# Kernel optimization log

Measured on AMD Instinct MI355X. Metric: run time of the kernel, lower is better.

Reference implementation:

```python
import jax, jax.numpy as jnp
import numpy as np

N = 100000   # nodes
E = 1600000  # edges (before self-loops)
F = 128      # in_dim
C = 32       # hidden_dim
H1 = 2       # heads of gat1
G = 64       # graphs in batch
NEG = 0.2    # leaky_relu slope (PyG default)


def segment_softmax(s, idx, num):
    # softmax of s grouped by idx (PyG `softmax`), s: [E, ...], idx: [E]
    m = jax.ops.segment_max(s, idx, num_segments=num)
    m = jnp.where(jnp.isfinite(m), m, 0.0)  # empty segments -> 0 baseline
    e = jnp.exp(s - m[idx])
    d = jax.ops.segment_sum(e, idx, num_segments=num)
    return e / (d[idx] + 1e-16)


def gatv2_layer(x, src, dst, Wl, bl, Wr, br, att, bias, heads, ch):
    # Faithful PyG GATv2Conv (share_weights=False, concat=True)
    n = x.shape[0]
    xl = (x @ Wl + bl).reshape(n, heads, ch)  # source transform
    xr = (x @ Wr + br).reshape(n, heads, ch)  # target transform
    e = jax.nn.leaky_relu(xl[src] + xr[dst], NEG)       # [E, H, C]
    alpha = jnp.sum(e * att, axis=-1)                    # [E, H]
    alpha = segment_softmax(alpha, dst, n)               # softmax over incoming edges
    out = jax.ops.segment_sum(alpha[..., None] * xl[src], dst, num_segments=n)
    return out.reshape(n, heads * ch) + bias


def setup_inputs() -> dict:
    key = jax.random.key(0)
    ks = jax.random.split(key, 24)
    s = 0.1
    inp = {
        "x": jax.random.normal(ks[0], (N, F), jnp.float32),
        "edge_index": jax.random.randint(ks[1], (2, E), 0, N),
        "batch": jnp.sort(jax.random.randint(ks[2], (N,), 0, G)),
        # gat1: in=F, heads=2, out=C
        "Wl1": jax.random.normal(ks[3], (F, H1 * C), jnp.float32) * s,
        "bl1": jnp.zeros((H1 * C,), jnp.float32),
        "Wr1": jax.random.normal(ks[4], (F, H1 * C), jnp.float32) * s,
        "br1": jnp.zeros((H1 * C,), jnp.float32),
        "att1": jax.random.normal(ks[5], (H1, C), jnp.float32) * s,
        "bias1": jnp.zeros((H1 * C,), jnp.float32),
        # gat2: in=2C, heads=1, out=C
        "Wl2": jax.random.normal(ks[6], (H1 * C, C), jnp.float32) * s,
        "bl2": jnp.zeros((C,), jnp.float32),
        "Wr2": jax.random.normal(ks[7], (H1 * C, C), jnp.float32) * s,
        "br2": jnp.zeros((C,), jnp.float32),
        "att2": jax.random.normal(ks[8], (1, C), jnp.float32) * s,
        "bias2": jnp.zeros((C,), jnp.float32),
        # gate_nn: Linear(C,C) -> ReLU -> Linear(C,1)
        "Wg1": jax.random.normal(ks[9], (C, C), jnp.float32) * s,
        "bg1": jnp.zeros((C,), jnp.float32),
        "Wg2": jax.random.normal(ks[10], (C, 1), jnp.float32) * s,
        "bg2": jnp.zeros((1,), jnp.float32),
        # head
        "W1": jax.random.normal(ks[11], (C, C), jnp.float32) * s,
        "b1": jnp.zeros((C,), jnp.float32),
        "W2": jax.random.normal(ks[12], (C, 1), jnp.float32) * s,
        "b2": jnp.zeros((1,), jnp.float32),
    }
    return inp


def reference(x, edge_index, batch,
              Wl1, bl1, Wr1, br1, att1, bias1,
              Wl2, bl2, Wr2, br2, att2, bias2,
              Wg1, bg1, Wg2, bg2, W1, b1, W2, b2):
    n = x.shape[0]
    ar = jnp.arange(n, dtype=edge_index.dtype)
    ei = jnp.concatenate([edge_index, jnp.stack([ar, ar])], axis=1)  # add self-loops
    src, dst = ei[0], ei[1]
    h = jax.nn.relu(gatv2_layer(x, src, dst, Wl1, bl1, Wr1, br1, att1, bias1, H1, C))
    h = jax.nn.relu(gatv2_layer(h, src, dst, Wl2, bl2, Wr2, br2, att2, bias2, 1, C))
    # GlobalAttention pooling
    gate = jax.nn.relu(h @ Wg1 + bg1) @ Wg2 + bg2   # [N, 1]
    a = segment_softmax(gate, batch, G)              # softmax per graph
    p = jax.ops.segment_sum(a * h, batch, num_segments=G)  # [G, C]
    o = jax.nn.relu(p @ W1 + b1) @ W2 + b2           # [G, 1]
    return o.squeeze(-1)
```

## Files before the change

kernel.cpp:

```cpp
#include <hip/hip_runtime.h>
#include <math.h>


constexpr float NEG_SLOPE = 0.2f;

typedef short bf16x8 __attribute__((ext_vector_type(8)));
typedef float f32x4  __attribute__((ext_vector_type(4)));

#define DPP_ADD(v, ctrl)                                                             \
  do {                                                                               \
    int _t = __builtin_amdgcn_update_dpp(0, __float_as_int(v), (ctrl), 0xF, 0xF, true); \
    (v) = (v) + __int_as_float(_t);                                                  \
  } while (0)
#define REDUCE4(v) do { DPP_ADD(v, 0xB1); DPP_ADD(v, 0x4E); } while (0)

__device__ __forceinline__ unsigned short f2bf(float f) {
  unsigned u = __float_as_uint(f);
  return (unsigned short)((u + 0x7FFFu + ((u >> 16) & 1u)) >> 16);
}
__device__ __forceinline__ float bf2f(unsigned short h) {
  return __uint_as_float(((unsigned)h) << 16);
}
__device__ __forceinline__ float bfLO(unsigned u) { return __uint_as_float(u << 16); }
__device__ __forceinline__ float bfHI(unsigned u) { return __uint_as_float(u & 0xFFFF0000u); }

__global__ __launch_bounds__(256) void wtrans_kernel(const float* __restrict__ Wl,
    const float* __restrict__ Wr, unsigned short* __restrict__ WT, int K, int NHALF)
{
  int groups = 2 * NHALF * (K / 8);
  for (int g = blockIdx.x * 256 + threadIdx.x; g < groups; g += gridDim.x * 256) {
    int col = g / (K / 8);
    int kb  = (g % (K / 8)) * 8;
    const float* W = (col < NHALF) ? Wl : Wr;
    int c = (col < NHALF) ? col : col - NHALF;
    float v[8];
#pragma unroll
    for (int i = 0; i < 8; ++i) v[i] = W[(size_t)(kb + i) * NHALF + c];
    ushort4 h0, h1;
    h0.x = f2bf(v[0]); h0.y = f2bf(v[1]); h0.z = f2bf(v[2]); h0.w = f2bf(v[3]);
    h1.x = f2bf(v[4]); h1.y = f2bf(v[5]); h1.z = f2bf(v[6]); h1.w = f2bf(v[7]);
    *(ushort4*)&WT[(size_t)col * K + kb]     = h0;
    *(ushort4*)&WT[(size_t)col * K + kb + 4] = h1;
  }
}

template<int K, int NHALF>
__global__ __launch_bounds__(256) void mm_mfma_kernel(const float* __restrict__ x,
    const unsigned short* __restrict__ WT,
    const float* __restrict__ bl, const float* __restrict__ br,
    unsigned short* __restrict__ outl, float* __restrict__ outr, int n)
{
  constexpr int NC = 2 * NHALF;
  constexpr int NT = NC / 16;
  constexpr int KC = K / 32;
  __shared__ unsigned short xs[64 * K];
  const int t = threadIdx.x;
  const int rowbase = blockIdx.x * 64;

  constexpr int GPT = (64 * K / 8) / 256;
#pragma unroll
  for (int g = 0; g < GPT; ++g) {
    int idx = t + g * 256;
    int row = idx / (K / 8);
    int kb  = (idx % (K / 8)) * 8;
    int grow = rowbase + row;
    float4 a0 = make_float4(0.f, 0.f, 0.f, 0.f), a1 = a0;
    if (grow < n) {
      a0 = *(const float4*)&x[(size_t)grow * K + kb];
      a1 = *(const float4*)&x[(size_t)grow * K + kb + 4];
    }
    ushort4 h0, h1;
    h0.x = f2bf(a0.x); h0.y = f2bf(a0.y); h0.z = f2bf(a0.z); h0.w = f2bf(a0.w);
    h1.x = f2bf(a1.x); h1.y = f2bf(a1.y); h1.z = f2bf(a1.z); h1.w = f2bf(a1.w);
    int ksw = kb ^ ((row & 7) << 3);
    *(ushort4*)&xs[row * K + ksw]     = h0;
    *(ushort4*)&xs[row * K + ksw + 4] = h1;
  }
  __syncthreads();

  const int w = t >> 6, l = t & 63;
  const int arow = w * 16 + (l & 15);
  const int kgrp = (l >> 4) * 8;
  const int asw  = (arow & 7) << 3;

  f32x4 zero = {0.f, 0.f, 0.f, 0.f};
  f32x4 acc[NT];
#pragma unroll
  for (int i = 0; i < NT; ++i) acc[i] = zero;

#pragma unroll
  for (int kc = 0; kc < KC; ++kc) {
    int k0 = kc * 32 + kgrp;
    bf16x8 a = *(const bf16x8*)&xs[arow * K + (k0 ^ asw)];
#pragma unroll
    for (int ct = 0; ct < NT; ++ct) {
      bf16x8 b = *(const bf16x8*)&WT[(size_t)(ct * 16 + (l & 15)) * K + k0];
      acc[ct] = __builtin_amdgcn_mfma_f32_16x16x32_bf16(a, b, acc[ct], 0, 0, 0);
    }
  }

  const int orow0 = rowbase + w * 16 + (l >> 4) * 4;
#pragma unroll
  for (int ct = 0; ct < NT; ++ct) {
    int c = ct * 16 + (l & 15);
    bool isl = c < NHALF;
    float bb = isl ? bl[c] : br[c - NHALF];
#pragma unroll
    for (int j = 0; j < 4; ++j) {
      int row = orow0 + j;
      if (row < n) {
        float v = acc[ct][j] + bb;
        if (isl) outl[(size_t)row * NHALF + c] = f2bf(v);
        else     outr[(size_t)row * NHALF + (c - NHALF)] = v;
      }
    }
  }
}

__global__ __launch_bounds__(256) void gate_kernel(const float* __restrict__ h2,
    const float* __restrict__ Wg1, const float* __restrict__ bg1,
    const float* __restrict__ Wg2, const float* __restrict__ bg2,
    float* __restrict__ gate, int n)
{
  int row = blockIdx.x * 256 + threadIdx.x;
  int rr = (row < n) ? row : 0;
  const float* hp = h2 + (size_t)rr * 32;
  float acc[32];
#pragma unroll
  for (int c = 0; c < 32; ++c) acc[c] = 0.f;
  for (int k0 = 0; k0 < 32; k0 += 8) {
    float4 a0 = *(const float4*)(hp + k0 + 0);
    float4 a1 = *(const float4*)(hp + k0 + 4);
    float xk[8];
    xk[0]=a0.x; xk[1]=a0.y; xk[2]=a0.z; xk[3]=a0.w;
    xk[4]=a1.x; xk[5]=a1.y; xk[6]=a1.z; xk[7]=a1.w;
#pragma unroll
    for (int kk = 0; kk < 8; ++kk) {
      const float* wv = Wg1 + (size_t)(k0 + kk) * 32;
#pragma unroll
      for (int c = 0; c < 32; ++c) acc[c] = fmaf(xk[kk], wv[c], acc[c]);
    }
  }
  if (row < n) {
    float g = 0.f;
#pragma unroll
    for (int c = 0; c < 32; ++c)
      g = fmaf(fmaxf(acc[c] + bg1[c], 0.f), Wg2[c], g);
    gate[row] = g + bg2[0];
  }
}

__global__ __launch_bounds__(256) void bucket_hist_kernel(const int* __restrict__ ei,
    int* __restrict__ buk_cnt, int E, int nbuk)
{
  __shared__ int h[512];
  for (int b = threadIdx.x; b < 512; b += 256) h[b] = 0;
  __syncthreads();
  int total = gridDim.x * 256;
  for (int i = blockIdx.x * 256 + threadIdx.x; i < E; i += total)
    atomicAdd(&h[((unsigned)ei[E + i]) >> 8], 1);
  __syncthreads();
  for (int b = threadIdx.x; b < nbuk; b += 256)
    if (h[b]) atomicAdd(&buk_cnt[b], h[b]);
}

__global__ __launch_bounds__(512) void scan_buckets_kernel(const int* __restrict__ buk_cnt,
    int* __restrict__ sbuk_off, int* __restrict__ buk_run, int nbuk, int E)
{
  __shared__ int lds[512];
  int t = threadIdx.x;
  int v = (t < nbuk) ? buk_cnt[t] : 0;
  lds[t] = v; __syncthreads();
  for (int off = 1; off < 512; off <<= 1) {
    int x = (t >= off) ? lds[t - off] : 0;
    __syncthreads();
    lds[t] += x;
    __syncthreads();
  }
  int excl = lds[t] - v;
  if (t < nbuk) { sbuk_off[t] = excl; buk_run[t] = excl; }
  if (t == nbuk) sbuk_off[t] = E;
}

__global__ __launch_bounds__(256) void partition_kernel(const int* __restrict__ ei,
    int* __restrict__ buk_run, unsigned* __restrict__ scratch, int E, int nbuk)
{
  __shared__ int lcnt[512];
  __shared__ int lbase[512];
  int t = threadIdx.x;
  for (int b = t; b < 512; b += 256) lcnt[b] = 0;
  __syncthreads();
  int chunk = (E + gridDim.x - 1) / gridDim.x;
  int s = blockIdx.x * chunk, e = min(E, s + chunk);
  for (int i = s + t; i < e; i += 256)
    atomicAdd(&lcnt[((unsigned)ei[E + i]) >> 8], 1);
  __syncthreads();
  for (int b = t; b < nbuk; b += 256) {
    int c = lcnt[b];
    lbase[b] = c ? atomicAdd(&buk_run[b], c) : 0;
    lcnt[b] = 0;
  }
  __syncthreads();
  for (int i = s + t; i < e; i += 256) {
    int src = ei[i];
    unsigned d = (unsigned)ei[E + i];
    int b = d >> 8;
    int r = atomicAdd(&lcnt[b], 1);
    scratch[lbase[b] + r] = (unsigned)src | ((d & 255u) << 17);
  }
}

__global__ __launch_bounds__(256) void bucket_fill_kernel(const unsigned* __restrict__ scratch,
    const int* __restrict__ sbuk_off, int* __restrict__ row_ptr,
    int* __restrict__ csr_src, int n, int nbuk)
{
  __shared__ int lcnt[256], sexcl[256], cnt2[256];
  int b = blockIdx.x, t = threadIdx.x;
  int dst0 = b << 8;
  int ndst = min(256, n - dst0);
  int s = sbuk_off[b], e = sbuk_off[b + 1];
  int base = s + dst0;
  lcnt[t] = (t < ndst) ? 1 : 0;
  __syncthreads();
  for (int i = s + t; i < e; i += 256)
    atomicAdd(&lcnt[scratch[i] >> 17], 1);
  __syncthreads();
  int c0 = lcnt[t];
  for (int off = 1; off < 256; off <<= 1) {
    int x = (t >= off) ? lcnt[t - off] : 0;
    __syncthreads();
    lcnt[t] += x;
    __syncthreads();
  }
  int ex = lcnt[t] - c0;
  sexcl[t] = ex;
  cnt2[t] = 1;
  if (t < ndst) {
    row_ptr[dst0 + t] = base + ex;
    csr_src[base + ex] = dst0 + t;
  }
  if (b == nbuk - 1 && t == 0) row_ptr[n] = sbuk_off[nbuk] + n;
  __syncthreads();
  for (int i = s + t; i < e; i += 256) {
    unsigned u = scratch[i];
    int dl = u >> 17;
    int src = u & 0x1FFFF;
    int pos = base + sexcl[dl] + atomicAdd(&cnt2[dl], 1);
    csr_src[pos] = src;
  }
}

__global__ __launch_bounds__(256) void gat1_kernel(const unsigned short* __restrict__ xl,
    const float* __restrict__ xr, const int* __restrict__ row_ptr,
    const int* __restrict__ csr_src, const float* __restrict__ att,
    const float* __restrict__ bias, float* __restrict__ hout, int n)
{
  int wid = (blockIdx.x * 256 + threadIdx.x) >> 6;
  if (wid >= n) return;
  wid = __builtin_amdgcn_readfirstlane(wid);
  int l = threadIdx.x & 63;
  int g8 = l >> 3;
  int q = l & 7;
  float xrv[8], attv[8], attn[8];
  {
    float4 x0 = *(const float4*)&xr[(size_t)wid * 64 + q * 8];
    float4 x1 = *(const float4*)&xr[(size_t)wid * 64 + q * 8 + 4];
    float4 a0 = *(const float4*)&att[q * 8];
    float4 a1 = *(const float4*)&att[q * 8 + 4];
    xrv[0]=x0.x; xrv[1]=x0.y; xrv[2]=x0.z; xrv[3]=x0.w;
    xrv[4]=x1.x; xrv[5]=x1.y; xrv[6]=x1.z; xrv[7]=x1.w;
    attv[0]=a0.x; attv[1]=a0.y; attv[2]=a0.z; attv[3]=a0.w;
    attv[4]=a1.x; attv[5]=a1.y; attv[6]=a1.z; attv[7]=a1.w;
#pragma unroll
    for (int i = 0; i < 8; ++i) attn[i] = attv[i] * NEG_SLOPE;
  }
  int s = row_ptr[wid], e = row_ptr[wid + 1];
  float acc[8];
#pragma unroll
  for (int i = 0; i < 8; ++i) acc[i] = 0.f;
  float d = 0.f;

#define LOAD1(CB, hv) {                                                       \
    int src_ = csr_src[min((CB) + g8, e - 1)];                                \
    hv = *(const int4*)&xl[(size_t)src_ * 64 + q * 8]; }

  int4 cur;
  LOAD1(s, cur)
  for (int cb = s; cb < e; cb += 8) {
    int4 nxt;
    LOAD1(min(cb + 8, e - 1), nxt)
    float xc[8];
    xc[0] = bfLO((unsigned)cur.x); xc[1] = bfHI((unsigned)cur.x);
    xc[2] = bfLO((unsigned)cur.y); xc[3] = bfHI((unsigned)cur.y);
    xc[4] = bfLO((unsigned)cur.z); xc[5] = bfHI((unsigned)cur.z);
    xc[6] = bfLO((unsigned)cur.w); xc[7] = bfHI((unsigned)cur.w);
    float v = 0.f;
#pragma unroll
    for (int i = 0; i < 8; ++i) {
      float t = xc[i] + xrv[i];
      v = fmaf(t, (t > 0.f) ? attv[i] : attn[i], v);
    }
    REDUCE4(v);
    float p = __expf(v);
    p = (cb + g8 < e) ? p : 0.f;
    d += p;
#pragma unroll
    for (int i = 0; i < 8; ++i) acc[i] = fmaf(p, xc[i], acc[i]);
    cur = nxt;
  }
#undef LOAD1
#pragma unroll
  for (int i = 0; i < 8; ++i) {
    acc[i] += __shfl_xor(acc[i], 8);
    acc[i] += __shfl_xor(acc[i], 16);
    acc[i] += __shfl_xor(acc[i], 32);
  }
  d += __shfl_xor(d, 8); d += __shfl_xor(d, 16); d += __shfl_xor(d, 32);
  if (g8 == 0) {
    float inv = 1.f / (d + 1e-16f);
    float4 b0 = *(const float4*)&bias[q * 8];
    float4 b1 = *(const float4*)&bias[q * 8 + 4];
    float4 o0, o1;
    o0.x = fmaxf(fmaf(acc[0], inv, b0.x), 0.f);
    o0.y = fmaxf(fmaf(acc[1], inv, b0.y), 0.f);
    o0.z = fmaxf(fmaf(acc[2], inv, b0.z), 0.f);
    o0.w = fmaxf(fmaf(acc[3], inv, b0.w), 0.f);
    o1.x = fmaxf(fmaf(acc[4], inv, b1.x), 0.f);
    o1.y = fmaxf(fmaf(acc[5], inv, b1.y), 0.f);
    o1.z = fmaxf(fmaf(acc[6], inv, b1.z), 0.f);
    o1.w = fmaxf(fmaf(acc[7], inv, b1.w), 0.f);
    *(float4*)&hout[(size_t)wid * 64 + q * 8]     = o0;
    *(float4*)&hout[(size_t)wid * 64 + q * 8 + 4] = o1;
  }
}

__global__ __launch_bounds__(256) void gat2_kernel(const unsigned short* __restrict__ xl,
    const float* __restrict__ xr, const int* __restrict__ row_ptr,
    const int* __restrict__ csr_src, const float* __restrict__ att,
    const float* __restrict__ bias, float* __restrict__ hout, int n)
{
  int wid = (blockIdx.x * 256 + threadIdx.x) >> 6;
  if (wid >= n) return;
  wid = __builtin_amdgcn_readfirstlane(wid);
  int l = threadIdx.x & 63;
  int g16 = l >> 2;
  int q = l & 3;
  float xrv[8], attv[8], attn[8];
  {
    float4 x0 = *(const float4*)&xr[(size_t)wid * 32 + q * 8];
    float4 x1 = *(const float4*)&xr[(size_t)wid * 32 + q * 8 + 4];
    float4 a0 = *(const float4*)&att[q * 8];
    float4 a1 = *(const float4*)&att[q * 8 + 4];
    xrv[0]=x0.x; xrv[1]=x0.y; xrv[2]=x0.z; xrv[3]=x0.w;
    xrv[4]=x1.x; xrv[5]=x1.y; xrv[6]=x1.z; xrv[7]=x1.w;
    attv[0]=a0.x; attv[1]=a0.y; attv[2]=a0.z; attv[3]=a0.w;
    attv[4]=a1.x; attv[5]=a1.y; attv[6]=a1.z; attv[7]=a1.w;
#pragma unroll
    for (int i = 0; i < 8; ++i) attn[i] = attv[i] * NEG_SLOPE;
  }
  int s = row_ptr[wid], e = row_ptr[wid + 1];
  int deg = e - s;
  float acc[8];
#pragma unroll
  for (int i = 0; i < 8; ++i) acc[i] = 0.f;
  float d = 0.f;

#define LOAD2(I0, hv) {                                                       \
    int src_ = csr_src[s + min((I0) + g16, deg - 1)];                         \
    hv = *(const int4*)&xl[(size_t)src_ * 32 + q * 8]; }

  int4 cur;
  LOAD2(0, cur)
  for (int i0 = 0; i0 < deg; i0 += 16) {
    int4 nxt;
    LOAD2(min(i0 + 16, deg - 1), nxt)
    float xc[8];
    xc[0] = bfLO((unsigned)cur.x); xc[1] = bfHI((unsigned)cur.x);
    xc[2] = bfLO((unsigned)cur.y); xc[3] = bfHI((unsigned)cur.y);
    xc[4] = bfLO((unsigned)cur.z); xc[5] = bfHI((unsigned)cur.z);
    xc[6] = bfLO((unsigned)cur.w); xc[7] = bfHI((unsigned)cur.w);
    float v = 0.f;
#pragma unroll
    for (int i = 0; i < 8; ++i) {
      float t = xc[i] + xrv[i];
      v = fmaf(t, (t > 0.f) ? attv[i] : attn[i], v);
    }
    REDUCE4(v);
    float p = __expf(v);
    p = (i0 + g16 < deg) ? p : 0.f;
    d += p;
#pragma unroll
    for (int i = 0; i < 8; ++i) acc[i] = fmaf(p, xc[i], acc[i]);
    cur = nxt;
  }
#undef LOAD2
#pragma unroll
  for (int i = 0; i < 8; ++i) {
    acc[i] += __shfl_xor(acc[i], 4);
    acc[i] += __shfl_xor(acc[i], 8);
    acc[i] += __shfl_xor(acc[i], 16);
    acc[i] += __shfl_xor(acc[i], 32);
  }
  d += __shfl_xor(d, 4); d += __shfl_xor(d, 8);
  d += __shfl_xor(d, 16); d += __shfl_xor(d, 32);
  if (g16 == 0) {
    float inv = 1.f / (d + 1e-16f);
    float4 b0 = *(const float4*)&bias[q * 8];
    float4 b1 = *(const float4*)&bias[q * 8 + 4];
    float4 o0, o1;
    o0.x = fmaxf(fmaf(acc[0], inv, b0.x), 0.f);
    o0.y = fmaxf(fmaf(acc[1], inv, b0.y), 0.f);
    o0.z = fmaxf(fmaf(acc[2], inv, b0.z), 0.f);
    o0.w = fmaxf(fmaf(acc[3], inv, b0.w), 0.f);
    o1.x = fmaxf(fmaf(acc[4], inv, b1.x), 0.f);
    o1.y = fmaxf(fmaf(acc[5], inv, b1.y), 0.f);
    o1.z = fmaxf(fmaf(acc[6], inv, b1.z), 0.f);
    o1.w = fmaxf(fmaf(acc[7], inv, b1.w), 0.f);
    *(float4*)&hout[(size_t)wid * 32 + q * 8]     = o0;
    *(float4*)&hout[(size_t)wid * 32 + q * 8 + 4] = o1;
  }
}

__global__ __launch_bounds__(1024) void pool_head_kernel(const float* __restrict__ h2,
    const float* __restrict__ gate, const int* __restrict__ batch,
    const float* __restrict__ W1, const float* __restrict__ b1,
    const float* __restrict__ W2, const float* __restrict__ b2,
    float* __restrict__ out, int n)
{
  int g = blockIdx.x;
  int t = threadIdx.x;
  int lo = 0, hi = n;
  while (lo < hi) { int mid = (lo + hi) >> 1; if (batch[mid] < g) lo = mid + 1; else hi = mid; }
  int s = lo;
  lo = s; hi = n;
  while (lo < hi) { int mid = (lo + hi) >> 1; if (batch[mid] < g + 1) lo = mid + 1; else hi = mid; }
  int e = lo;

  __shared__ float red[1024];
  float lm = -INFINITY;
  for (int i = s + t; i < e; i += 1024) lm = fmaxf(lm, gate[i]);
  red[t] = lm; __syncthreads();
  for (int off = 512; off > 0; off >>= 1) {
    if (t < off) red[t] = fmaxf(red[t], red[t + off]);
    __syncthreads();
  }
  float m = (s == e) ? 0.f : red[0];
  __syncthreads();

  int c = t & 31, grp = t >> 5;
  float acc = 0.f, dsum = 0.f;
  for (int i = s + grp; i < e; i += 32) {
    float sv = __expf(gate[i] - m);
    acc += sv * h2[(size_t)i * 32 + c];
    if (c == 0) dsum += sv;
  }
  __shared__ float accs[32][33];
  __shared__ float dss[32];
  accs[grp][c] = acc;
  if (c == 0) dss[grp] = dsum;
  __syncthreads();

  if (t < 32) {
    float a = 0.f, dd = 0.f;
#pragma unroll
    for (int k = 0; k < 32; ++k) { a += accs[k][t]; dd += dss[k]; }
    float p = a / (dd + 1e-16f);
    float q = 0.f;
    for (int cc = 0; cc < 32; ++cc)
      q = fmaf(__shfl(p, cc, 32), W1[cc * 32 + t], q);
    q = fmaxf(q + b1[t], 0.f);
    float r = q * W2[t];
    r += __shfl_xor(r, 1, 32);  r += __shfl_xor(r, 2, 32);
    r += __shfl_xor(r, 4, 32);  r += __shfl_xor(r, 8, 32);
    r += __shfl_xor(r, 16, 32);
    if (t == 0) out[g] = r + b2[0];
  }
}

extern "C" void kernel_launch(void* const* d_in, const int* in_sizes, int n_in,
                              void* d_out, int out_size, void* d_ws, size_t ws_size,
                              hipStream_t stream)
{
  const float* x     = (const float*)d_in[0];
  const int*   ei    = (const int*)d_in[1];
  const int*   batch = (const int*)d_in[2];
  const float* Wl1   = (const float*)d_in[3];
  const float* bl1   = (const float*)d_in[4];
  const float* Wr1   = (const float*)d_in[5];
  const float* br1   = (const float*)d_in[6];
  const float* att1  = (const float*)d_in[7];
  const float* bias1 = (const float*)d_in[8];
  const float* Wl2   = (const float*)d_in[9];
  const float* bl2   = (const float*)d_in[10];
  const float* Wr2   = (const float*)d_in[11];
  const float* br2   = (const float*)d_in[12];
  const float* att2  = (const float*)d_in[13];
  const float* bias2 = (const float*)d_in[14];
  const float* Wg1   = (const float*)d_in[15];
  const float* bg1   = (const float*)d_in[16];
  const float* Wg2   = (const float*)d_in[17];
  const float* bg2   = (const float*)d_in[18];
  const float* W1    = (const float*)d_in[19];
  const float* b1    = (const float*)d_in[20];
  const float* W2    = (const float*)d_in[21];
  const float* b2    = (const float*)d_in[22];
  float* out = (float*)d_out;

  const int n = in_sizes[2];
  const int E = in_sizes[1] / 2;
  const int Etot = E + n;
  const int nbuk = (n + 255) / 256;

  float* fws = (float*)d_ws;
  size_t nf64 = (size_t)n * 64;
  float* bufA = fws;
  float* bufB = bufA + nf64;
  float* bufC = bufB + nf64;
  unsigned short* xl1 = (unsigned short*)bufA;
  float* xr1 = bufB;
  float* hbuf = bufC;
  unsigned short* xl2 = (unsigned short*)bufA;
  float* xr2 = bufA + (size_t)n * 16;
  float* h2  = bufB;
  float* gate = bufB + (size_t)n * 32;
  unsigned* scratch = (unsigned*)bufC;
  int* ip       = (int*)(bufC + nf64);
  int* row_ptr  = ip;  ip += (n + 2);
  int* buk_cnt  = ip;  ip += 512;
  int* sbuk_off = ip;  ip += 520;
  int* buk_run  = ip;  ip += 512;
  int* csr_src  = ip;  ip += Etot;
  unsigned short* WT1 = (unsigned short*)ip;
  unsigned short* WT2 = WT1 + 128 * 128;

  hipMemsetAsync(buk_cnt, 0, 512 * sizeof(int), stream);

  int mb64 = (n + 63) / 64;

  wtrans_kernel<<<8, 256, 0, stream>>>(Wl1, Wr1, WT1, 128, 64);
  wtrans_kernel<<<2, 256, 0, stream>>>(Wl2, Wr2, WT2, 64, 32);

  mm_mfma_kernel<128, 64><<<mb64, 256, 0, stream>>>(x, WT1, bl1, br1, xl1, xr1, n);

  bucket_hist_kernel<<<256, 256, 0, stream>>>(ei, buk_cnt, E, nbuk);
  scan_buckets_kernel<<<1, 512, 0, stream>>>(buk_cnt, sbuk_off, buk_run, nbuk, E);
  partition_kernel<<<256, 256, 0, stream>>>(ei, buk_run, scratch, E, nbuk);
  bucket_fill_kernel<<<nbuk, 256, 0, stream>>>(scratch, sbuk_off, row_ptr, csr_src, n, nbuk);

  int gatblocks = (n + 3) / 4;
  gat1_kernel<<<gatblocks, 256, 0, stream>>>(xl1, xr1, row_ptr, csr_src, att1, bias1, hbuf, n);

  mm_mfma_kernel<64, 32><<<mb64, 256, 0, stream>>>(hbuf, WT2, bl2, br2, xl2, xr2, n);

  gat2_kernel<<<gatblocks, 256, 0, stream>>>(xl2, xr2, row_ptr, csr_src, att2, bias2, h2, n);

  gate_kernel<<<(n + 255) / 256, 256, 0, stream>>>(h2, Wg1, bg1, Wg2, bg2, gate, n);

  pool_head_kernel<<<64, 1024, 0, stream>>>(h2, gate, batch, W1, b1, W2, b2, out, n);
}
```

Measured before the change: 254.5 us.

## Remap MFMA GEMM waves to column tiles with register-resident weights; branchless leaky-relu

The projection GEMM now assigns each wave one 16-column tile and iterates over the four 16-row tiles. The weight fragments are loaded once into registers instead of being re-read from global memory for every row tile. The first-layer GEMM launches 8 waves per block to cover its 128 output columns. Separately, the GAT attention scores compute leaky_relu·att as 0.6·att·t + 0.4·att·|t|, removing the per-element select at the cost of one extra FMA. That identity is exact only for slope 0.2, up to floating-point rounding.

```diff
diff --git a/kernel.cpp b/kernel.cpp
--- a/kernel.cpp
+++ b/kernel.cpp
@@ -17,9 +17,6 @@
 __device__ __forceinline__ unsigned short f2bf(float f) {
   unsigned u = __float_as_uint(f);
   return (unsigned short)((u + 0x7FFFu + ((u >> 16) & 1u)) >> 16);
-}
-__device__ __forceinline__ float bf2f(unsigned short h) {
-  return __uint_as_float(((unsigned)h) << 16);
 }
 __device__ __forceinline__ float bfLO(unsigned u) { return __uint_as_float(u << 16); }
 __device__ __forceinline__ float bfHI(unsigned u) { return __uint_as_float(u & 0xFFFF0000u); }
@@ -44,23 +41,30 @@
   }
 }
 
-template<int K, int NHALF>
-__global__ __launch_bounds__(256) void mm_mfma_kernel(const float* __restrict__ x,
+template<int K, int NHALF, int WAVES>
+__global__ __launch_bounds__(WAVES * 64) void mm_mfma_kernel(const float* __restrict__ x,
     const unsigned short* __restrict__ WT,
     const float* __restrict__ bl, const float* __restrict__ br,
     unsigned short* __restrict__ outl, float* __restrict__ outr, int n)
 {
-  constexpr int NC = 2 * NHALF;
-  constexpr int NT = NC / 16;
   constexpr int KC = K / 32;
+  constexpr int NT_THREADS = WAVES * 64;
   __shared__ unsigned short xs[64 * K];
   const int t = threadIdx.x;
   const int rowbase = blockIdx.x * 64;
-
-  constexpr int GPT = (64 * K / 8) / 256;
+  const int w = t >> 6, l = t & 63;
+  const int bcol = w * 16 + (l & 15);
+  const int kgrp = (l >> 4) * 8;
+
+  bf16x8 bfr[KC];
+#pragma unroll
+  for (int kc = 0; kc < KC; ++kc)
+    bfr[kc] = *(const bf16x8*)&WT[(size_t)bcol * K + kc * 32 + kgrp];
+
+  constexpr int GPT = (64 * K / 8) / NT_THREADS;
 #pragma unroll
   for (int g = 0; g < GPT; ++g) {
-    int idx = t + g * 256;
+    int idx = t + g * NT_THREADS;
     int row = idx / (K / 8);
     int kb  = (idx % (K / 8)) * 8;
     int grow = rowbase + row;
@@ -78,40 +82,35 @@
   }
   __syncthreads();
 
-  const int w = t >> 6, l = t & 63;
-  const int arow = w * 16 + (l & 15);
-  const int kgrp = (l >> 4) * 8;
-  const int asw  = (arow & 7) << 3;
-
   f32x4 zero = {0.f, 0.f, 0.f, 0.f};
-  f32x4 acc[NT];
-#pragma unroll
-  for (int i = 0; i < NT; ++i) acc[i] = zero;
-
-#pragma unroll
-  for (int kc = 0; kc < KC; ++kc) {
-    int k0 = kc * 32 + kgrp;
-    bf16x8 a = *(const bf16x8*)&xs[arow * K + (k0 ^ asw)];
-#pragma unroll
-    for (int ct = 0; ct < NT; ++ct) {
-      bf16x8 b = *(const bf16x8*)&WT[(size_t)(ct * 16 + (l & 15)) * K + k0];
-      acc[ct] = __builtin_amdgcn_mfma_f32_16x16x32_bf16(a, b, acc[ct], 0, 0, 0);
+  f32x4 acc[4];
+#pragma unroll
+  for (int i = 0; i < 4; ++i) acc[i] = zero;
+
+#pragma unroll
+  for (int rt = 0; rt < 4; ++rt) {
+    int arow = rt * 16 + (l & 15);
+    int asw  = (arow & 7) << 3;
+#pragma unroll
+    for (int kc = 0; kc < KC; ++kc) {
+      bf16x8 a = *(const bf16x8*)&xs[arow * K + ((kc * 32 + kgrp) ^ asw)];
+      acc[rt] = __builtin_amdgcn_mfma_f32_16x16x32_bf16(a, bfr[kc], acc[rt], 0, 0, 0);
     }
   }
 
-  const int orow0 = rowbase + w * 16 + (l >> 4) * 4;
-#pragma unroll
-  for (int ct = 0; ct < NT; ++ct) {
-    int c = ct * 16 + (l & 15);
-    bool isl = c < NHALF;
-    float bb = isl ? bl[c] : br[c - NHALF];
+  const bool isl = bcol < NHALF;
+  const int col = isl ? bcol : bcol - NHALF;
+  const float bb = isl ? bl[col] : br[col];
+#pragma unroll
+  for (int rt = 0; rt < 4; ++rt) {
+    int r0 = rowbase + rt * 16 + (l >> 4) * 4;
 #pragma unroll
     for (int j = 0; j < 4; ++j) {
-      int row = orow0 + j;
+      int row = r0 + j;
       if (row < n) {
-        float v = acc[ct][j] + bb;
-        if (isl) outl[(size_t)row * NHALF + c] = f2bf(v);
-        else     outr[(size_t)row * NHALF + (c - NHALF)] = v;
+        float v = acc[rt][j] + bb;
+        if (isl) outl[(size_t)row * NHALF + col] = f2bf(v);
+        else     outr[(size_t)row * NHALF + col] = v;
       }
     }
   }
@@ -261,18 +260,19 @@
   int l = threadIdx.x & 63;
   int g8 = l >> 3;
   int q = l & 7;
-  float xrv[8], attv[8], attn[8];
+  float xrv[8], a6[8], a4[8];
   {
     float4 x0 = *(const float4*)&xr[(size_t)wid * 64 + q * 8];
     float4 x1 = *(const float4*)&xr[(size_t)wid * 64 + q * 8 + 4];
-    float4 a0 = *(const float4*)&att[q * 8];
-    float4 a1 = *(const float4*)&att[q * 8 + 4];
+    float4 c0 = *(const float4*)&att[q * 8];
+    float4 c1 = *(const float4*)&att[q * 8 + 4];
     xrv[0]=x0.x; xrv[1]=x0.y; xrv[2]=x0.z; xrv[3]=x0.w;
     xrv[4]=x1.x; xrv[5]=x1.y; xrv[6]=x1.z; xrv[7]=x1.w;
-    attv[0]=a0.x; attv[1]=a0.y; attv[2]=a0.z; attv[3]=a0.w;
-    attv[4]=a1.x; attv[5]=a1.y; attv[6]=a1.z; attv[7]=a1.w;
-#pragma unroll
-    for (int i = 0; i < 8; ++i) attn[i] = attv[i] * NEG_SLOPE;
+    float av[8];
+    av[0]=c0.x; av[1]=c0.y; av[2]=c0.z; av[3]=c0.w;
+    av[4]=c1.x; av[5]=c1.y; av[6]=c1.z; av[7]=c1.w;
+#pragma unroll
+    for (int i = 0; i < 8; ++i) { a6[i] = 0.6f * av[i]; a4[i] = 0.4f * av[i]; }
   }
   int s = row_ptr[wid], e = row_ptr[wid + 1];
   float acc[8];
@@ -298,7 +298,8 @@
 #pragma unroll
     for (int i = 0; i < 8; ++i) {
       float t = xc[i] + xrv[i];
-      v = fmaf(t, (t > 0.f) ? attv[i] : attn[i], v);
+      v = fmaf(t, a6[i], v);
+      v = fmaf(fabsf(t), a4[i], v);
     }
     REDUCE4(v);
     float p = __expf(v);
@@ -345,18 +346,19 @@
   int l = threadIdx.x & 63;
   int g16 = l >> 2;
   int q = l & 3;
-  float xrv[8], attv[8], attn[8];
+  float xrv[8], a6[8], a4[8];
   {
     float4 x0 = *(const float4*)&xr[(size_t)wid * 32 + q * 8];
     float4 x1 = *(const float4*)&xr[(size_t)wid * 32 + q * 8 + 4];
-    float4 a0 = *(const float4*)&att[q * 8];
-    float4 a1 = *(const float4*)&att[q * 8 + 4];
+    float4 c0 = *(const float4*)&att[q * 8];
+    float4 c1 = *(const float4*)&att[q * 8 + 4];
     xrv[0]=x0.x; xrv[1]=x0.y; xrv[2]=x0.z; xrv[3]=x0.w;
     xrv[4]=x1.x; xrv[5]=x1.y; xrv[6]=x1.z; xrv[7]=x1.w;
-    attv[0]=a0.x; attv[1]=a0.y; attv[2]=a0.z; attv[3]=a0.w;
-    attv[4]=a1.x; attv[5]=a1.y; attv[6]=a1.z; attv[7]=a1.w;
-#pragma unroll
-    for (int i = 0; i < 8; ++i) attn[i] = attv[i] * NEG_SLOPE;
+    float av[8];
+    av[0]=c0.x; av[1]=c0.y; av[2]=c0.z; av[3]=c0.w;
+    av[4]=c1.x; av[5]=c1.y; av[6]=c1.z; av[7]=c1.w;
+#pragma unroll
+    for (int i = 0; i < 8; ++i) { a6[i] = 0.6f * av[i]; a4[i] = 0.4f * av[i]; }
   }
   int s = row_ptr[wid], e = row_ptr[wid + 1];
   int deg = e - s;
@@ -383,7 +385,8 @@
 #pragma unroll
     for (int i = 0; i < 8; ++i) {
       float t = xc[i] + xrv[i];
-      v = fmaf(t, (t > 0.f) ? attv[i] : attn[i], v);
+      v = fmaf(t, a6[i], v);
+      v = fmaf(fabsf(t), a4[i], v);
     }
     REDUCE4(v);
     float p = __expf(v);
@@ -540,7 +543,7 @@
   wtrans_kernel<<<8, 256, 0, stream>>>(Wl1, Wr1, WT1, 128, 64);
   wtrans_kernel<<<2, 256, 0, stream>>>(Wl2, Wr2, WT2, 64, 32);
 
-  mm_mfma_kernel<128, 64><<<mb64, 256, 0, stream>>>(x, WT1, bl1, br1, xl1, xr1, n);
+  mm_mfma_kernel<128, 64, 8><<<mb64, 512, 0, stream>>>(x, WT1, bl1, br1, xl1, xr1, n);
 
   bucket_hist_kernel<<<256, 256, 0, stream>>>(ei, buk_cnt, E, nbuk);
   scan_buckets_kernel<<<1, 512, 0, stream>>>(buk_cnt, sbuk_off, buk_run, nbuk, E);
@@ -550,7 +553,7 @@
   int gatblocks = (n + 3) / 4;
   gat1_kernel<<<gatblocks, 256, 0, stream>>>(xl1, xr1, row_ptr, csr_src, att1, bias1, hbuf, n);
 
-  mm_mfma_kernel<64, 32><<<mb64, 256, 0, stream>>>(hbuf, WT2, bl2, br2, xl2, xr2, n);
+  mm_mfma_kernel<64, 32, 4><<<mb64, 256, 0, stream>>>(hbuf, WT2, bl2, br2, xl2, xr2, n);
 
   gat2_kernel<<<gatblocks, 256, 0, stream>>>(xl2, xr2, row_ptr, csr_src, att2, bias2, h2, n);
 
```

Result: faster. 223.2 us (-12.3%).
